# Kernel tuning notes

Hardware: AMD Instinct MI355X
Metric: run time of the kernel (lower is better)

Reference implementation:

```python
import jax, jax.numpy as jnp
import numpy as np

N_ATOMS = 256
N_FEATURES = 128
BATCH = 8
BINS = 300


def _segments(n, length=1):
    # all pairs of non-overlapping length-`length` segments: rows [i, i+L, j, j+L], j >= i+L+1
    m = n - length
    i, j = np.triu_indices(m, k=length + 1)
    return np.stack([i, i + length, j, j + length], axis=1).astype(np.int32)  # (Nseg, 4)


SEGMENTS_NP = _segments(N_ATOMS)
NSEG = SEGMENTS_NP.shape[0]  # 32131 for n_atoms=256
# edges: segment start-pairs and end-pairs, shape (2, 2*Nseg), then offset per frame
_edges_base = np.concatenate([SEGMENTS_NP[:, [0, 2]], SEGMENTS_NP[:, [1, 3]]], axis=0).T
EDGES_NP = np.concatenate([b * N_ATOMS + _edges_base for b in range(BATCH)], axis=1)  # (2, B*2*Nseg)
SRC = jnp.asarray(EDGES_NP[0].astype(np.int32))
DST = jnp.asarray(EDGES_NP[1].astype(np.int32))
SEGMENTS = jnp.asarray(SEGMENTS_NP)
BIN_CENTERS = jnp.linspace(-1.0, 1.0, BINS, dtype=jnp.float32)
STEP = 2.0 / (BINS - 1)  # linear (non-gaussian) binning: scalar step


def _divnorm(x):
    return x / jnp.linalg.norm(x, axis=-1, keepdims=True)


def _writhe_segments_cross(xyz, seg):
    # xyz: (B, N, 3), seg: (S, 4) -> writhe per segment pair (B, S)
    B, S = xyz.shape[0], seg.shape[0]
    # dx[b, s, k]: broadcasted differences xyz[seg[2+q]] - xyz[seg[p]], k = 2*p+q
    dx = (-xyz[:, seg[:, :2], None] + xyz[:, seg[:, None, 2:]]).reshape(B, S, 4, 3)
    dx = _divnorm(dx)
    crosses = _divnorm(jnp.cross(dx[:, :, [0, 1, 3, 2]], dx[:, :, [1, 3, 2, 0]]))
    dots = jnp.clip(jnp.sum(crosses * crosses[:, :, [1, 2, 3, 0]], axis=-1), -1.0, 1.0)
    omega = jnp.arcsin(dots).sum(axis=2)  # (B, S)
    signs = jnp.sign(jnp.sum(
        jnp.cross(xyz[:, seg[:, 3]] - xyz[:, seg[:, 2]], xyz[:, seg[:, 1]] - xyz[:, seg[:, 0]]) * dx[:, :, 0],
        axis=-1))
    return omega * signs / (2.0 * jnp.pi)


def setup_inputs() -> dict:
    key = jax.random.key(0)
    k1, k2, k3 = jax.random.split(key, 3)
    coords = jax.random.normal(k1, (BATCH * N_ATOMS, 3), jnp.float32)
    node_features = jax.random.normal(k2, (BATCH * N_ATOMS, N_FEATURES), jnp.float32)
    std = 1.0 / np.sqrt(N_FEATURES)
    basis = jax.random.uniform(k3, (BINS, N_FEATURES), jnp.float32, -std, std)
    return {"coords": coords, "node_features": node_features, "basis": basis}


def reference(coords, node_features, basis):
    xyz = coords.reshape(BATCH, N_ATOMS, 3)
    wr = _writhe_segments_cross(xyz, SEGMENTS)  # (B, Nseg)
    # Gaussian RBF soft one-hot over linear bins, then project onto learned basis
    enc = jnp.exp(-(((wr[..., None] - BIN_CENTERS) / STEP) ** 2)) / 1.12  # (B, S, bins)
    emb = jnp.einsum('bsk,kf->bsf', enc, basis)  # (B, S, F)
    # repeat(1,2,1): each segment pair contributes two edges (start-pair, end-pair)
    writhe_feat = jnp.tile(emb, (1, 2, 1)).reshape(-1, N_FEATURES)  # (B*2S, F)
    # distance attention: exp(-||r_src - r_dst||^2), softmax-normalized per destination node
    w = jnp.exp(-jnp.sum((coords[SRC] - coords[DST]) ** 2, axis=-1))  # (E,)
    denom = jax.ops.segment_sum(w, DST, num_segments=BATCH * N_ATOMS)
    attn = (w / denom[DST])[:, None]
    message = jax.ops.segment_sum(writhe_feat * attn, DST, num_segments=BATCH * N_ATOMS)
    return node_features + message
```

## Files before the change

kernel.cpp:

```cpp
#include <hip/hip_runtime.h>
#include <math.h>

#define N_ATOMS 256
#define N_FEAT  128
#define BATCH   8
#define BINS    300
#define INV_STEP 149.5f
#define ONE_OVER_2PI 0.15915494309189535f
#define INV_112 0.8928571428571429f
#define WIN 2
#define WINW 5
#define NHIST 8
#define EXPM2 0.13533528323661270f

struct V3 { float x, y, z; };
__device__ __forceinline__ V3 v3sub(V3 a, V3 b) { return {a.x-b.x, a.y-b.y, a.z-b.z}; }
__device__ __forceinline__ float v3dot(V3 a, V3 b) { return a.x*b.x + a.y*b.y + a.z*b.z; }
__device__ __forceinline__ V3 v3cross(V3 a, V3 b) {
    return {a.y*b.z - a.z*b.y, a.z*b.x - a.x*b.z, a.x*b.y - a.y*b.x};
}
__device__ __forceinline__ float clamp1(float x) { return fminf(1.0f, fmaxf(-1.0f, x)); }

__device__ __forceinline__ float asin_fast(float x) {
    float u = fabsf(x);
    bool big = u > 0.5f;
    float z = big ? 0.5f * (1.0f - u) : u * u;
    float s = big ? __builtin_amdgcn_sqrtf(z) : u;
    float p = fmaf(z, 4.2163199048e-2f, 2.4181311049e-2f);
    p = fmaf(z, p, 4.5470025998e-2f);
    p = fmaf(z, p, 7.4953002686e-2f);
    p = fmaf(z, p, 1.6666752422e-1f);
    float r = fmaf(s * z, p, s);
    r = big ? (1.5707963267948966f - 2.0f * r) : r;
    return copysignf(r, x);
}

__device__ __forceinline__ float writhe_ij(const float4* cs, int i, int j) {
    const float4 qi  = cs[i],   qi1 = cs[i + 1];
    const float4 qj  = cs[j],   qj1 = cs[j + 1];
    V3 pi  = {qi.x,  qi.y,  qi.z};
    V3 pi1 = {qi1.x, qi1.y, qi1.z};
    V3 pj  = {qj.x,  qj.y,  qj.z};
    V3 pj1 = {qj1.x, qj1.y, qj1.z};

    V3 u0 = v3sub(pj,  pi);
    V3 u1 = v3sub(pj1, pi);
    V3 u2 = v3sub(pj,  pi1);
    V3 u3 = v3sub(pj1, pi1);

    V3 c0 = v3cross(u0, u1);
    V3 c1 = v3cross(u1, u3);
    V3 c2 = v3cross(u3, u2);
    V3 c3 = v3cross(u2, u0);

    float r0 = __builtin_amdgcn_rsqf(v3dot(c0, c0));
    float r1 = __builtin_amdgcn_rsqf(v3dot(c1, c1));
    float r2 = __builtin_amdgcn_rsqf(v3dot(c2, c2));
    float r3 = __builtin_amdgcn_rsqf(v3dot(c3, c3));

    float omega = asin_fast(clamp1(v3dot(c0, c1) * (r0 * r1)))
                + asin_fast(clamp1(v3dot(c1, c2) * (r1 * r2)))
                + asin_fast(clamp1(v3dot(c2, c3) * (r2 * r3)))
                + asin_fast(clamp1(v3dot(c3, c0) * (r3 * r0)));

    float sg = v3dot(v3cross(v3sub(pj1, pj), v3sub(pi1, pi)), u0);
    float sign = (sg > 0.0f) ? 1.0f : ((sg < 0.0f) ? -1.0f : 0.0f);
    return omega * sign * ONE_OVER_2PI;
}

__global__ __launch_bounds__(512) void fused_kernel(const float* __restrict__ coords,
                                                    const float* __restrict__ nf,
                                                    const float* __restrict__ basis,
                                                    float* __restrict__ out) {
    const int blk = blockIdx.x;
    const int b = blk & 7;
    const int p = blk >> 3;
    const int t0 = p + 2;
    const int t1 = 255 - p;
    const int tid = threadIdx.x;

    const int E0  = 2 * t0 - 3;
    const int E1n = (t1 == 255) ? 253 : 2 * t1 - 3;

    float mynf = 0.0f;
    if (tid < 256) {
        const int row = (tid >> 7) ? t1 : t0;
        mynf = nf[((size_t)((b << 8) | row)) * N_FEAT + (tid & 127)];
    }

    __shared__ float4 cs[N_ATOMS];
    __shared__ float h2[2 * NHIST * BINS];
    __shared__ float part[4 * N_FEAT];
    __shared__ float sden[2];
    __shared__ int skmin[2], skmax[2];

    if (tid < N_ATOMS) {
        const int gbase = ((b << 8) + tid) * 3;
        cs[tid] = make_float4(coords[gbase], coords[gbase + 1], coords[gbase + 2], 0.0f);
    }
    if (tid < 2) { sden[tid] = 0.0f; skmin[tid] = BINS - 1; skmax[tid] = 0; }
    __syncthreads();

    int node = -1;
    int tau = t0;
    if (tid < E0) { node = 0; tau = t0; }
    else if (tid < E0 + E1n) { node = 1; tau = t1; }
    const int ee = (node == 1) ? tid - E0 : tid;

    float g = 0.0f, pp = 0.0f;
    int k0 = 0;
    float d0 = 0.0f, d1 = 0.0f;
    int kn0 = BINS - 1, kx0 = 0, kn1 = BINS - 1, kx1 = 0;

    if (node >= 0) {
        const int eT1 = (tau <= N_ATOMS - 2) ? tau - 1 : 0;
        const int typ = (ee < eT1) ? 0 : 1;
        const int a = (typ == 0) ? ee : ee - eT1 + 1;

        const float4 qa = cs[a];
        const float4 qt = cs[tau];
        float dx = qa.x - qt.x;
        float dy = qa.y - qt.y;
        float dz = qa.z - qt.z;
        g = __expf(-(dx*dx + dy*dy + dz*dz));

        float w = writhe_ij(cs, a - typ, tau - typ);
        pp = (w + 1.0f) * INV_STEP;
        k0 = __float2int_rn(pp);
        int kmn = max(0, k0 - WIN);
        int kmx = min(BINS - 1, k0 + WIN);
        if (node == 0) { d0 = g; kn0 = kmn; kx0 = kmx; }
        else           { d1 = g; kn1 = kmn; kx1 = kmx; }
    }

    #pragma unroll
    for (int off = 32; off > 0; off >>= 1) {
        d0 += __shfl_xor(d0, off, 64);
        d1 += __shfl_xor(d1, off, 64);
        kn0 = min(kn0, __shfl_xor(kn0, off, 64));
        kx0 = max(kx0, __shfl_xor(kx0, off, 64));
        kn1 = min(kn1, __shfl_xor(kn1, off, 64));
        kx1 = max(kx1, __shfl_xor(kx1, off, 64));
    }
    if ((tid & 63) == 0) {
        atomicAdd(&sden[0], d0);
        atomicAdd(&sden[1], d1);
        atomicMin(&skmin[0], kn0);
        atomicMax(&skmax[0], kx0);
        atomicMin(&skmin[1], kn1);
        atomicMax(&skmax[1], kx1);
    }
    __syncthreads();

    {
        const int nu = tid >> 8;
        const int l = tid & 255;
        const int kmin = skmin[nu], kmax = skmax[nu];
        const int base = nu * NHIST * BINS;
        for (int k = kmin + l; k <= kmax; k += 256) {
            #pragma unroll
            for (int c = 0; c < NHIST; ++c) h2[base + c * BINS + k] = 0.0f;
        }
    }
    __syncthreads();

    if (node >= 0) {
        const int base = (node * NHIST + (tid & (NHIST - 1))) * BINS;
        const int klo = k0 - WIN;
        float d = pp - (float)klo;
        float e = g * __expf(-d * d);
        float u = __expf(2.0f * d - 1.0f);
        #pragma unroll
        for (int m = 0; m < WINW; ++m) {
            const int k = klo + m;
            if (k >= 0 && k < BINS) atomicAdd(&h2[base + k], e);
            e *= u;
            u *= EXPM2;
        }
    }
    __syncthreads();

    {
        const int nu = tid >> 8;
        const int kmin = skmin[nu], kmax = skmax[nu];
        const int base = nu * NHIST * BINS;
        for (int k = kmin + (tid & 255); k <= kmax; k += 256) {
            float s = h2[base + k];
            #pragma unroll
            for (int c = 1; c < NHIST; ++c) s += h2[base + c * BINS + k];
            h2[base + k] = s;
        }
    }
    __syncthreads();

    {
        const int nu = tid >> 8;
        const int h = (tid >> 7) & 1;
        const int f = tid & 127;
        const int kmin = skmin[nu], kmax = skmax[nu];
        const int len = kmax - kmin + 1;
        const int half = (len + 1) >> 1;
        const int ks = kmin + h * half;
        const int ke = min(kmax + 1, ks + half);
        const int base = nu * NHIST * BINS;
        float acc = 0.0f;
        for (int k = ks; k < ke; ++k)
            acc = fmaf(h2[base + k], basis[k * N_FEAT + f], acc);
        part[((nu << 1) | h) * N_FEAT + f] = acc;
    }
    __syncthreads();

    if (tid < 256) {
        const int nu = tid >> 7;
        const int f = tid & 127;
        const int row = nu ? t1 : t0;
        const float scale = INV_112 / sden[nu];
        const float s = part[(nu << 1) * N_FEAT + f] + part[((nu << 1) | 1) * N_FEAT + f];
        out[((size_t)((b << 8) | row)) * N_FEAT + f] = mynf + s * scale;
    } else if (p == 0) {
        const int tid2 = tid - 256;
        const int r = tid2 >> 7;
        const int f = tid2 & 127;
        const size_t idx = ((size_t)((b << 8) | r)) * N_FEAT + f;
        out[idx] = nf[idx];
    }
}

extern "C" void kernel_launch(void* const* d_in, const int* in_sizes, int n_in,
                              void* d_out, int out_size, void* d_ws, size_t ws_size,
                              hipStream_t stream) {
    const float* coords = (const float*)d_in[0];
    const float* nf     = (const float*)d_in[1];
    const float* basis  = (const float*)d_in[2];
    float* out = (float*)d_out;

    fused_kernel<<<BATCH * 127, 512, 0, stream>>>(coords, nf, basis, out);
}
```

Measured before the change: 103.2 us.

## Halve block size to 256 threads with two edges per thread

The block shrinks from 512 to 256 threads. Each thread now computes up to two edges (its own plus tid+256 for the second node), which removes the idle upper half of the old block. Histogram copies drop from 8 to 4. The basis projection is no longer split into halves with a shared partial-sum stage; each thread does the full bin range with two accumulators, which saves one barrier. This trades more work per thread and more atomic contention on fewer histogram copies for better thread utilisation and more resident blocks.

```diff
diff --git a/kernel.cpp b/kernel.cpp
--- a/kernel.cpp
+++ b/kernel.cpp
@@ -10,7 +10,7 @@
 #define INV_112 0.8928571428571429f
 #define WIN 2
 #define WINW 5
-#define NHIST 8
+#define NHIST 4
 #define EXPM2 0.13533528323661270f
 
 struct V3 { float x, y, z; };
@@ -68,7 +68,25 @@
     return omega * sign * ONE_OVER_2PI;
 }
 
-__global__ __launch_bounds__(512) void fused_kernel(const float* __restrict__ coords,
+__device__ __forceinline__ void edge_compute(const float4* cs, int tau, int ee,
+                                             float& g, float& pp, int& k0) {
+    const int eT1 = (tau <= N_ATOMS - 2) ? tau - 1 : 0;
+    const int typ = (ee < eT1) ? 0 : 1;
+    const int a = (typ == 0) ? ee : ee - eT1 + 1;
+
+    const float4 qa = cs[a];
+    const float4 qt = cs[tau];
+    const float dx = qa.x - qt.x;
+    const float dy = qa.y - qt.y;
+    const float dz = qa.z - qt.z;
+    g = __expf(-(dx*dx + dy*dy + dz*dz));
+
+    const float w = writhe_ij(cs, a - typ, tau - typ);
+    pp = (w + 1.0f) * INV_STEP;
+    k0 = __float2int_rn(pp);
+}
+
+__global__ __launch_bounds__(256) void fused_kernel(const float* __restrict__ coords,
                                                     const float* __restrict__ nf,
                                                     const float* __restrict__ basis,
                                                     float* __restrict__ out) {
@@ -81,56 +99,48 @@
 
     const int E0  = 2 * t0 - 3;
     const int E1n = (t1 == 255) ? 253 : 2 * t1 - 3;
-
-    float mynf = 0.0f;
-    if (tid < 256) {
-        const int row = (tid >> 7) ? t1 : t0;
-        mynf = nf[((size_t)((b << 8) | row)) * N_FEAT + (tid & 127)];
-    }
+    const int E = E0 + E1n;
+
+    const int nu_out = tid >> 7;
+    const int f_out = tid & 127;
+    const int row_out = nu_out ? t1 : t0;
+    const float mynf = nf[((size_t)((b << 8) | row_out)) * N_FEAT + f_out];
 
     __shared__ float4 cs[N_ATOMS];
     __shared__ float h2[2 * NHIST * BINS];
-    __shared__ float part[4 * N_FEAT];
     __shared__ float sden[2];
     __shared__ int skmin[2], skmax[2];
 
-    if (tid < N_ATOMS) {
+    {
         const int gbase = ((b << 8) + tid) * 3;
         cs[tid] = make_float4(coords[gbase], coords[gbase + 1], coords[gbase + 2], 0.0f);
     }
     if (tid < 2) { sden[tid] = 0.0f; skmin[tid] = BINS - 1; skmax[tid] = 0; }
     __syncthreads();
 
-    int node = -1;
-    int tau = t0;
-    if (tid < E0) { node = 0; tau = t0; }
-    else if (tid < E0 + E1n) { node = 1; tau = t1; }
-    const int ee = (node == 1) ? tid - E0 : tid;
-
-    float g = 0.0f, pp = 0.0f;
-    int k0 = 0;
-    float d0 = 0.0f, d1 = 0.0f;
+    const bool act1 = (tid < E);
+    const int node1e = (tid < E0) ? 0 : 1;
+    const int ee1 = (node1e == 1) ? min(tid - E0, E1n - 1) : tid;
+    const int tau1 = node1e ? t1 : t0;
+
+    const bool act2 = (tid + 256 < E);
+    const int ee2 = act2 ? (tid + 256 - E0) : 0;
+
+    float g1, pp1; int k01;
+    float g2, pp2; int k02;
+    edge_compute(cs, tau1, ee1, g1, pp1, k01);
+    edge_compute(cs, t1,   ee2, g2, pp2, k02);
+
+    float d0 = (act1 && node1e == 0) ? g1 : 0.0f;
+    float d1 = ((act1 && node1e == 1) ? g1 : 0.0f) + (act2 ? g2 : 0.0f);
     int kn0 = BINS - 1, kx0 = 0, kn1 = BINS - 1, kx1 = 0;
-
-    if (node >= 0) {
-        const int eT1 = (tau <= N_ATOMS - 2) ? tau - 1 : 0;
-        const int typ = (ee < eT1) ? 0 : 1;
-        const int a = (typ == 0) ? ee : ee - eT1 + 1;
-
-        const float4 qa = cs[a];
-        const float4 qt = cs[tau];
-        float dx = qa.x - qt.x;
-        float dy = qa.y - qt.y;
-        float dz = qa.z - qt.z;
-        g = __expf(-(dx*dx + dy*dy + dz*dz));
-
-        float w = writhe_ij(cs, a - typ, tau - typ);
-        pp = (w + 1.0f) * INV_STEP;
-        k0 = __float2int_rn(pp);
-        int kmn = max(0, k0 - WIN);
-        int kmx = min(BINS - 1, k0 + WIN);
-        if (node == 0) { d0 = g; kn0 = kmn; kx0 = kmx; }
-        else           { d1 = g; kn1 = kmn; kx1 = kmx; }
+    if (act1) {
+        const int kmn = max(0, k01 - WIN), kmx = min(BINS - 1, k01 + WIN);
+        if (node1e == 0) { kn0 = kmn; kx0 = kmx; } else { kn1 = kmn; kx1 = kmx; }
+    }
+    if (act2) {
+        kn1 = min(kn1, max(0, k02 - WIN));
+        kx1 = max(kx1, min(BINS - 1, k02 + WIN));
     }
 
     #pragma unroll
@@ -153,22 +163,23 @@
     __syncthreads();
 
     {
-        const int nu = tid >> 8;
-        const int l = tid & 255;
+        const int nu = tid >> 7;
+        const int l = tid & 127;
         const int kmin = skmin[nu], kmax = skmax[nu];
         const int base = nu * NHIST * BINS;
-        for (int k = kmin + l; k <= kmax; k += 256) {
+        for (int k = kmin + l; k <= kmax; k += 128) {
             #pragma unroll
             for (int c = 0; c < NHIST; ++c) h2[base + c * BINS + k] = 0.0f;
         }
     }
     __syncthreads();
 
-    if (node >= 0) {
-        const int base = (node * NHIST + (tid & (NHIST - 1))) * BINS;
-        const int klo = k0 - WIN;
-        float d = pp - (float)klo;
-        float e = g * __expf(-d * d);
+    const int copy = tid & (NHIST - 1);
+    if (act1) {
+        const int base = (node1e * NHIST + copy) * BINS;
+        const int klo = k01 - WIN;
+        float d = pp1 - (float)klo;
+        float e = g1 * __expf(-d * d);
         float u = __expf(2.0f * d - 1.0f);
         #pragma unroll
         for (int m = 0; m < WINW; ++m) {
@@ -178,50 +189,48 @@
             u *= EXPM2;
         }
     }
-    __syncthreads();
-
-    {
-        const int nu = tid >> 8;
+    if (act2) {
+        const int base = (NHIST + copy) * BINS;
+        const int klo = k02 - WIN;
+        float d = pp2 - (float)klo;
+        float e = g2 * __expf(-d * d);
+        float u = __expf(2.0f * d - 1.0f);
+        #pragma unroll
+        for (int m = 0; m < WINW; ++m) {
+            const int k = klo + m;
+            if (k >= 0 && k < BINS) atomicAdd(&h2[base + k], e);
+            e *= u;
+            u *= EXPM2;
+        }
+    }
+    __syncthreads();
+
+    {
+        const int nu = tid >> 7;
         const int kmin = skmin[nu], kmax = skmax[nu];
         const int base = nu * NHIST * BINS;
-        for (int k = kmin + (tid & 255); k <= kmax; k += 256) {
-            float s = h2[base + k];
-            #pragma unroll
-            for (int c = 1; c < NHIST; ++c) s += h2[base + c * BINS + k];
-            h2[base + k] = s;
-        }
-    }
-    __syncthreads();
-
-    {
-        const int nu = tid >> 8;
-        const int h = (tid >> 7) & 1;
-        const int f = tid & 127;
-        const int kmin = skmin[nu], kmax = skmax[nu];
-        const int len = kmax - kmin + 1;
-        const int half = (len + 1) >> 1;
-        const int ks = kmin + h * half;
-        const int ke = min(kmax + 1, ks + half);
-        const int base = nu * NHIST * BINS;
-        float acc = 0.0f;
-        for (int k = ks; k < ke; ++k)
-            acc = fmaf(h2[base + k], basis[k * N_FEAT + f], acc);
-        part[((nu << 1) | h) * N_FEAT + f] = acc;
-    }
-    __syncthreads();
-
-    if (tid < 256) {
-        const int nu = tid >> 7;
-        const int f = tid & 127;
-        const int row = nu ? t1 : t0;
-        const float scale = INV_112 / sden[nu];
-        const float s = part[(nu << 1) * N_FEAT + f] + part[((nu << 1) | 1) * N_FEAT + f];
-        out[((size_t)((b << 8) | row)) * N_FEAT + f] = mynf + s * scale;
-    } else if (p == 0) {
-        const int tid2 = tid - 256;
-        const int r = tid2 >> 7;
-        const int f = tid2 & 127;
-        const size_t idx = ((size_t)((b << 8) | r)) * N_FEAT + f;
+        for (int k = kmin + (tid & 127); k <= kmax; k += 128) {
+            h2[base + k] = h2[base + k] + h2[base + BINS + k]
+                         + h2[base + 2 * BINS + k] + h2[base + 3 * BINS + k];
+        }
+    }
+    __syncthreads();
+
+    {
+        const int kmin = skmin[nu_out], kmax = skmax[nu_out];
+        const int base = nu_out * NHIST * BINS;
+        float acc0 = 0.0f, acc1 = 0.0f;
+        int k = kmin;
+        for (; k + 1 <= kmax; k += 2) {
+            acc0 = fmaf(h2[base + k],     basis[k * N_FEAT + f_out],       acc0);
+            acc1 = fmaf(h2[base + k + 1], basis[(k + 1) * N_FEAT + f_out], acc1);
+        }
+        if (k <= kmax) acc0 = fmaf(h2[base + k], basis[k * N_FEAT + f_out], acc0);
+        out[((size_t)((b << 8) | row_out)) * N_FEAT + f_out]
+            = mynf + (acc0 + acc1) * (INV_112 / sden[nu_out]);
+    }
+    if (p == 0) {
+        const size_t idx = ((size_t)((b << 8) | nu_out)) * N_FEAT + f_out;
         out[idx] = nf[idx];
     }
 }
@@ -234,5 +243,5 @@
     const float* basis  = (const float*)d_in[2];
     float* out = (float*)d_out;
 
-    fused_kernel<<<BATCH * 127, 512, 0, stream>>>(coords, nf, basis, out);
-}
+    fused_kernel<<<BATCH * 127, 256, 0, stream>>>(coords, nf, basis, out);
+}
```

Result: faster. 99.33 us (-3.8%).
